# Kernel optimization log

Measured on AMD Instinct MI355X. Metric: run time of the kernel, lower is better.

The kernel has to match this reference:

```python
import jax, jax.numpy as jnp
import numpy as np

B, S, D = 1, 2048, 4096
H, DN, DR, DV = 16, 128, 64, 128        # heads, nope dim, rope dim, v dim
QLORA, KVLORA = 1536, 512
IN_, ID_, TOPK = 16, 128, 1024          # indexer heads, indexer head dim, top-k
NEG = -1e30


def _rope_interleaved(x, cos, sin):
    # pairs (x0,x1) interleaved as complex: used for MLA q/k rope parts
    xr, xi = x[..., 0::2], x[..., 1::2]
    yr = xr * cos - xi * sin
    yi = xr * sin + xi * cos
    return jnp.stack([yr, yi], axis=-1).reshape(x.shape)


def _rope_noninterleaved(x, cos, sin):
    # first half real, second half imaginary (indexer rope)
    h = x.shape[-1] // 2
    xr, xi = x[..., :h], x[..., h:]
    return jnp.concatenate([xr * cos - xi * sin, xr * sin + xi * cos], axis=-1)


def _rmsnorm(x, w, eps=1e-6):
    v = jnp.mean(jnp.square(x), axis=-1, keepdims=True)
    return x * jax.lax.rsqrt(v + eps) * w


def _layernorm(x, w, b, eps=1e-5):
    mu = jnp.mean(x, axis=-1, keepdims=True)
    var = jnp.mean(jnp.square(x - mu), axis=-1, keepdims=True)
    return (x - mu) * jax.lax.rsqrt(var + eps) * w + b


def setup_inputs() -> dict:
    key = jax.random.key(0)
    ks = jax.random.split(key, 9)
    def w(k, shape):
        return jax.random.normal(k, shape, jnp.float32) * 0.02
    hidden_states = jax.random.normal(ks[0], (B, S, D), jnp.float32)
    w_q_a = w(ks[1], (D, QLORA))
    w_q_b = w(ks[2], (QLORA, H * (DN + DR)))
    w_kv_a = w(ks[3], (D, KVLORA + DR))
    w_kv_b = w(ks[4], (KVLORA, H * (DN + DV)))
    w_o = w(ks[5], (H * DV, D))
    idx_wq_b = w(ks[6], (QLORA, IN_ * ID_))
    idx_wk = w(ks[7], (D, ID_))
    idx_w_proj = w(ks[8], (D, IN_))
    q_a_ln_w = jnp.ones((QLORA,), jnp.float32)
    kv_a_ln_w = jnp.ones((KVLORA,), jnp.float32)
    idx_k_ln_w = jnp.ones((ID_,), jnp.float32)
    idx_k_ln_b = jnp.zeros((ID_,), jnp.float32)
    inv_freq = 1.0 / (10000.0 ** (np.arange(0, DR, 2) / DR))
    ang = np.arange(S)[:, None] * inv_freq[None, :]  # [S, DR//2]
    cos = jnp.asarray(np.cos(ang), jnp.float32)
    sin = jnp.asarray(np.sin(ang), jnp.float32)
    return dict(hidden_states=hidden_states, cos=cos, sin=sin, w_q_a=w_q_a,
                q_a_ln_w=q_a_ln_w, w_q_b=w_q_b, w_kv_a=w_kv_a, kv_a_ln_w=kv_a_ln_w,
                w_kv_b=w_kv_b, w_o=w_o, idx_wq_b=idx_wq_b, idx_wk=idx_wk,
                idx_k_ln_w=idx_k_ln_w, idx_k_ln_b=idx_k_ln_b, idx_w_proj=idx_w_proj)


def reference(hidden_states, cos, sin, w_q_a, q_a_ln_w, w_q_b, w_kv_a, kv_a_ln_w,
              w_kv_b, w_o, idx_wq_b, idx_wk, idx_k_ln_w, idx_k_ln_b, idx_w_proj):
    b, s, _ = hidden_states.shape
    cos3, sin3 = cos[None, :, :], sin[None, :, :]          # [1, s, DR/2]
    cos4, sin4 = cos[None, :, None, :], sin[None, :, None, :]  # per-head broadcast

    # ---- MLA projections ----
    cq = _rmsnorm(hidden_states @ w_q_a, q_a_ln_w)          # [b,s,QLORA]
    q = (cq @ w_q_b).reshape(b, s, H, DN + DR)
    q_nope, q_rope = q[..., :DN], q[..., DN:]
    q_rope = _rope_interleaved(q_rope, cos4, sin4)
    kv = hidden_states @ w_kv_a                             # [b,s,KVLORA+DR]
    kv_c = _rmsnorm(kv[..., :KVLORA], kv_a_ln_w)
    k_rope = _rope_interleaved(kv[..., KVLORA:], cos3, sin3)  # shared (MQA) [b,s,DR]
    kvb = (kv_c @ w_kv_b).reshape(b, s, H, DN + DV)
    k_nope, v = kvb[..., :DN], kvb[..., DN:]

    causal = jnp.tril(jnp.ones((s, s), bool))

    # ---- lightning indexer (top-k token selection) ----
    qi = (cq @ idx_wq_b).reshape(b, s, IN_, ID_)
    qi = jnp.concatenate([_rope_noninterleaved(qi[..., :DR], cos4, sin4), qi[..., DR:]], -1)
    ki = _layernorm(hidden_states @ idx_wk, idx_k_ln_w, idx_k_ln_b)  # [b,s,ID_]
    ki = jnp.concatenate([_rope_noninterleaved(ki[..., :DR], cos3, sin3), ki[..., DR:]], -1)
    # NOTE: hadamard_transform_activation falls back to identity (no package) -> identity here
    wts = (hidden_states @ idx_w_proj) * (IN_ ** -0.5)       # [b,s,IN_]
    iscores = jax.nn.relu(jnp.einsum('bqnd,bkd->bqnk', qi, ki) * (ID_ ** -0.5))
    iscores = jnp.einsum('bqnk,bqn->bqk', iscores, wts)
    iscores = jnp.where(causal[None], iscores, NEG)
    _, topk_idx = jax.lax.top_k(iscores, TOPK)               # [b,s,TOPK]
    topk_mask = jnp.zeros((b, s, s), bool).at[
        jnp.arange(b)[:, None, None], jnp.arange(s)[None, :, None], topk_idx].set(True)
    allowed = topk_mask & causal[None]                       # [b,s,s]

    # ---- sparse MLA attention ----
    scale = (DN + DR) ** -0.5
    scores = (jnp.einsum('bqhd,bkhd->bhqk', q_nope, k_nope)
              + jnp.einsum('bqhd,bkd->bhqk', q_rope, k_rope)) * scale
    scores = jnp.where(allowed[:, None], scores, NEG)
    probs = jax.nn.softmax(scores, axis=-1)
    attn = jnp.einsum('bhqk,bkhd->bqhd', probs, v)
    return attn.reshape(b, s, H * DV) @ w_o
```

## Files before the change

kernel.cpp:

```cpp
#include <hip/hip_runtime.h>
#include <math.h>

#define S_LEN 2048
#define D_MODEL 4096
#define NH 16
#define TOPK_ 1024

typedef float f32x4 __attribute__((ext_vector_type(4)));
typedef short bf16x8 __attribute__((ext_vector_type(8)));

__device__ __forceinline__ unsigned short f2bf(float f) {
  unsigned u = __float_as_uint(f);
  u += 0x7fffu + ((u >> 16) & 1u);
  return (unsigned short)(u >> 16);
}

__device__ __forceinline__ void gload16(const unsigned short* g, unsigned short* l) {
  __builtin_amdgcn_global_load_lds(
      (const __attribute__((address_space(1))) unsigned int*)g,
      (__attribute__((address_space(3))) unsigned int*)l, 16, 0, 0);
}

__global__ __launch_bounds__(256) void gemm_bf16x(const unsigned short* __restrict__ A,
                                                  const unsigned short* __restrict__ Bt,
                                                  float* __restrict__ C,
                                                  int K, int lda, int ldb, int ldc,
                                                  int za, int zb, int zc) {
  A += (size_t)blockIdx.z * za;
  Bt += (size_t)blockIdx.z * zb;
  C += (size_t)blockIdx.z * zc;
  __shared__ __align__(16) unsigned short As[128 * 32];
  __shared__ __align__(16) unsigned short Bs[128 * 32];
  const int t = threadIdx.x, lane = t & 63, w = t >> 6;
  const int m0 = blockIdx.y * 128, n0 = blockIdx.x * 128;
  const int mb = (w & 1) * 64, nb = (w >> 1) * 64;
  const int fr = lane & 15, fq = lane >> 4;
  f32x4 acc[4][4];
#pragma unroll
  for (int i = 0; i < 4; i++)
#pragma unroll
    for (int j = 0; j < 4; j++) acc[i][j] = (f32x4){0.f, 0.f, 0.f, 0.f};
  const int grow = t >> 2, gsub = (t & 3) * 8;
  unsigned short* aswL = &As[w * 512];
  unsigned short* aswH = &As[2048 + w * 512];
  unsigned short* bswL = &Bs[w * 512];
  unsigned short* bswH = &Bs[2048 + w * 512];
  const unsigned short* AgL = A + (size_t)(m0 + grow) * lda + gsub;
  const unsigned short* AgH = A + (size_t)(m0 + 64 + grow) * lda + gsub;
  const unsigned short* BgL = Bt + (size_t)(n0 + grow) * ldb + gsub;
  const unsigned short* BgH = Bt + (size_t)(n0 + 64 + grow) * ldb + gsub;
  for (int k0 = 0; k0 < K; k0 += 32) {
    __syncthreads();
    gload16(AgL + k0, aswL);
    gload16(AgH + k0, aswH);
    gload16(BgL + k0, bswL);
    gload16(BgH + k0, bswH);
    __syncthreads();
    bf16x8 af[4], bfr[4];
#pragma unroll
    for (int mt = 0; mt < 4; mt++) af[mt] = *(const bf16x8*)&As[(mb + mt * 16 + fr) * 32 + fq * 8];
#pragma unroll
    for (int nt = 0; nt < 4; nt++) bfr[nt] = *(const bf16x8*)&Bs[(nb + nt * 16 + fr) * 32 + fq * 8];
#pragma unroll
    for (int mt = 0; mt < 4; mt++)
#pragma unroll
      for (int nt = 0; nt < 4; nt++)
        acc[mt][nt] = __builtin_amdgcn_mfma_f32_16x16x32_bf16(af[mt], bfr[nt], acc[mt][nt], 0, 0, 0);
  }
#pragma unroll
  for (int mt = 0; mt < 4; mt++) {
#pragma unroll
    for (int r = 0; r < 4; r++) {
      int row = m0 + mb + mt * 16 + fq * 4 + r;
      float* cp = C + (size_t)row * ldc + n0 + nb + fr;
#pragma unroll
      for (int nt = 0; nt < 4; nt++) cp[nt * 16] = acc[mt][nt][r];
    }
  }
}

__global__ __launch_bounds__(256) void gemm_bf16x_bf(const unsigned short* __restrict__ A,
                                                     const unsigned short* __restrict__ Bt,
                                                     unsigned short* __restrict__ C,
                                                     int K, int lda, int ldb, int ldc,
                                                     int za, int zb, int zc, float scale) {
  A += (size_t)blockIdx.z * za;
  Bt += (size_t)blockIdx.z * zb;
  C += (size_t)blockIdx.z * zc;
  __shared__ __align__(16) unsigned short As[128 * 32];
  __shared__ __align__(16) unsigned short Bs[128 * 32];
  const int t = threadIdx.x, lane = t & 63, w = t >> 6;
  const int m0 = blockIdx.y * 128, n0 = blockIdx.x * 128;
  const int mb = (w & 1) * 64, nb = (w >> 1) * 64;
  const int fr = lane & 15, fq = lane >> 4;
  f32x4 acc[4][4];
#pragma unroll
  for (int i = 0; i < 4; i++)
#pragma unroll
    for (int j = 0; j < 4; j++) acc[i][j] = (f32x4){0.f, 0.f, 0.f, 0.f};
  const int grow = t >> 2, gsub = (t & 3) * 8;
  unsigned short* aswL = &As[w * 512];
  unsigned short* aswH = &As[2048 + w * 512];
  unsigned short* bswL = &Bs[w * 512];
  unsigned short* bswH = &Bs[2048 + w * 512];
  const unsigned short* AgL = A + (size_t)(m0 + grow) * lda + gsub;
  const unsigned short* AgH = A + (size_t)(m0 + 64 + grow) * lda + gsub;
  const unsigned short* BgL = Bt + (size_t)(n0 + grow) * ldb + gsub;
  const unsigned short* BgH = Bt + (size_t)(n0 + 64 + grow) * ldb + gsub;
  for (int k0 = 0; k0 < K; k0 += 32) {
    __syncthreads();
    gload16(AgL + k0, aswL);
    gload16(AgH + k0, aswH);
    gload16(BgL + k0, bswL);
    gload16(BgH + k0, bswH);
    __syncthreads();
    bf16x8 af[4], bfr[4];
#pragma unroll
    for (int mt = 0; mt < 4; mt++) af[mt] = *(const bf16x8*)&As[(mb + mt * 16 + fr) * 32 + fq * 8];
#pragma unroll
    for (int nt = 0; nt < 4; nt++) bfr[nt] = *(const bf16x8*)&Bs[(nb + nt * 16 + fr) * 32 + fq * 8];
#pragma unroll
    for (int mt = 0; mt < 4; mt++)
#pragma unroll
      for (int nt = 0; nt < 4; nt++)
        acc[mt][nt] = __builtin_amdgcn_mfma_f32_16x16x32_bf16(af[mt], bfr[nt], acc[mt][nt], 0, 0, 0);
  }
#pragma unroll
  for (int mt = 0; mt < 4; mt++) {
#pragma unroll
    for (int r = 0; r < 4; r++) {
      int row = m0 + mb + mt * 16 + fq * 4 + r;
      unsigned short* cp = C + (size_t)row * ldc + n0 + nb + fr;
#pragma unroll
      for (int nt = 0; nt < 4; nt++) cp[nt * 16] = f2bf(acc[mt][nt][r] * scale);
    }
  }
}

__global__ __launch_bounds__(256) void cast_bf16(const float* __restrict__ in,
                                                 unsigned short* __restrict__ out) {
  size_t i = (size_t)(blockIdx.x * 256 + threadIdx.x) * 8;
  float4 v0 = *(const float4*)(in + i);
  float4 v1 = *(const float4*)(in + i + 4);
  unsigned short tmp[8] = {f2bf(v0.x), f2bf(v0.y), f2bf(v0.z), f2bf(v0.w),
                           f2bf(v1.x), f2bf(v1.y), f2bf(v1.z), f2bf(v1.w)};
  *(float4*)(out + i) = *(float4*)tmp;
}

__global__ __launch_bounds__(256) void transpose_cast(const float* __restrict__ in,
                                                      unsigned short* __restrict__ out,
                                                      int K, int N) {
  __shared__ float buf[64][33];
  const int k0 = blockIdx.y * 64, n0 = blockIdx.x * 32;
  const int t = threadIdx.x;
  const bool valid = (n0 < N);
  if (valid) {
#pragma unroll
    for (int i = 0; i < 2; i++) {
      int c = i * 256 + t;
      int kk = c >> 3, nn = (c & 7) * 4;
      float4 v = *(const float4*)(in + (size_t)(k0 + kk) * N + n0 + nn);
      buf[kk][nn] = v.x; buf[kk][nn + 1] = v.y; buf[kk][nn + 2] = v.z; buf[kk][nn + 3] = v.w;
    }
  }
  __syncthreads();
  const int n = t >> 3, k8 = (t & 7) * 8;
  unsigned short tmp[8];
#pragma unroll
  for (int j = 0; j < 8; j++) tmp[j] = valid ? f2bf(buf[k8 + j][n]) : (unsigned short)0;
  *(float4*)(out + (size_t)(n0 + n) * K + k0 + k8) = *(float4*)tmp;
}

__global__ __launch_bounds__(256) void transpose_wv(const unsigned short* __restrict__ wkvbbf,
                                                    unsigned short* __restrict__ wvT) {
  __shared__ unsigned short tile[128][136];
  const int c0 = blockIdx.x * 128, h = blockIdx.y;
  const int t = threadIdx.x;
  for (int i = t; i < 128 * 16; i += 256) {
    int c = i >> 4, sub = (i & 15) * 8;
    *(float4*)&tile[c][sub] = *(const float4*)(wkvbbf + (size_t)(c0 + c) * 4096 + h * 256 + 128 + sub);
  }
  __syncthreads();
  for (int i = t; i < 128 * 16; i += 256) {
    int d = i >> 4, cs = (i & 15) * 8;
    unsigned short tmp[8];
#pragma unroll
    for (int j = 0; j < 8; j++) tmp[j] = tile[cs + j][d];
    *(float4*)(wvT + (size_t)h * 65536 + (size_t)d * 512 + c0 + cs) = *(float4*)tmp;
  }
}

__global__ __launch_bounds__(256) void rmsnorm_kernel(float* __restrict__ x,
                                                      const float* __restrict__ w,
                                                      int ncol, int stride) {
  const int s = blockIdx.x, t = threadIdx.x;
  float* row = x + (size_t)s * stride;
  float ss = 0.f;
  for (int d = t; d < ncol; d += 256) { float v = row[d]; ss += v * v; }
  __shared__ float red[256];
  red[t] = ss;
  __syncthreads();
  for (int o = 128; o > 0; o >>= 1) { if (t < o) red[t] += red[t + o]; __syncthreads(); }
  float r = 1.0f / sqrtf(red[0] / (float)ncol + 1e-6f);
  for (int d = t; d < ncol; d += 256) row[d] = row[d] * r * w[d];
}

__global__ __launch_bounds__(256) void rmsnorm_bf16_kernel(float* __restrict__ x,
                                                           const float* __restrict__ w,
                                                           unsigned short* __restrict__ xbf,
                                                           int ncol, int stride) {
  const int s = blockIdx.x, t = threadIdx.x;
  float* row = x + (size_t)s * stride;
  float ss = 0.f;
  for (int d = t; d < ncol; d += 256) { float v = row[d]; ss += v * v; }
  __shared__ float red[256];
  red[t] = ss;
  __syncthreads();
  for (int o = 128; o > 0; o >>= 1) { if (t < o) red[t] += red[t + o]; __syncthreads(); }
  float r = 1.0f / sqrtf(red[0] / (float)ncol + 1e-6f);
  for (int d = t; d < ncol; d += 256) {
    float v = row[d] * r * w[d];
    row[d] = v;
    xbf[(size_t)s * ncol + d] = f2bf(v);
  }
}

__global__ __launch_bounds__(128) void layernorm128_kernel(float* __restrict__ x,
                                                           const float* __restrict__ w,
                                                           const float* __restrict__ b) {
  const int s = blockIdx.x, t = threadIdx.x;
  float* row = x + (size_t)s * 128;
  __shared__ float red[128];
  float v = row[t];
  red[t] = v;
  __syncthreads();
  for (int o = 64; o > 0; o >>= 1) { if (t < o) red[t] += red[t + o]; __syncthreads(); }
  float mu = red[0] / 128.f;
  __syncthreads();
  float d = v - mu;
  red[t] = d * d;
  __syncthreads();
  for (int o = 64; o > 0; o >>= 1) { if (t < o) red[t] += red[t + o]; __syncthreads(); }
  float var = red[0] / 128.f;
  row[t] = d * (1.0f / sqrtf(var + 1e-5f)) * w[t] + b[t];
}

__global__ __launch_bounds__(256) void rope_q_inter(float* __restrict__ q,
                                                    const float* __restrict__ cosp,
                                                    const float* __restrict__ sinp) {
  int id = blockIdx.x * 256 + threadIdx.x;
  int s = id >> 9, r = id & 511, h = r >> 5, j = r & 31;
  float c = cosp[s * 32 + j], sn = sinp[s * 32 + j];
  float* base = q + (size_t)s * (NH * 192) + h * 192 + 128 + 2 * j;
  float x0 = base[0], x1 = base[1];
  base[0] = x0 * c - x1 * sn;
  base[1] = x0 * sn + x1 * c;
}

__global__ __launch_bounds__(256) void rope_k_inter(float* __restrict__ kv,
                                                    const float* __restrict__ cosp,
                                                    const float* __restrict__ sinp,
                                                    int stride) {
  int id = blockIdx.x * 256 + threadIdx.x;
  int s = id >> 5, j = id & 31;
  float c = cosp[s * 32 + j], sn = sinp[s * 32 + j];
  float* base = kv + (size_t)s * stride + 512 + 2 * j;
  float x0 = base[0], x1 = base[1];
  base[0] = x0 * c - x1 * sn;
  base[1] = x0 * sn + x1 * c;
}

__global__ __launch_bounds__(256) void rope_qi_nonint(float* __restrict__ qi,
                                                      const float* __restrict__ cosp,
                                                      const float* __restrict__ sinp) {
  int id = blockIdx.x * 256 + threadIdx.x;
  int s = id >> 9, r = id & 511, n = r >> 5, j = r & 31;
  float c = cosp[s * 32 + j], sn = sinp[s * 32 + j];
  float* base = qi + (size_t)s * 2048 + n * 128;
  float xr = base[j], xi = base[j + 32];
  base[j] = xr * c - xi * sn;
  base[j + 32] = xr * sn + xi * c;
}

__global__ __launch_bounds__(256) void rope_ki_nonint(float* __restrict__ ki,
                                                      const float* __restrict__ cosp,
                                                      const float* __restrict__ sinp) {
  int id = blockIdx.x * 256 + threadIdx.x;
  int s = id >> 5, j = id & 31;
  float c = cosp[s * 32 + j], sn = sinp[s * 32 + j];
  float* base = ki + (size_t)s * 128;
  float xr = base[j], xi = base[j + 32];
  base[j] = xr * c - xi * sn;
  base[j + 32] = xr * sn + xi * c;
}

__global__ __launch_bounds__(256) void wts_kernel(const float* __restrict__ hs,
                                                  const float* __restrict__ wp,
                                                  float* __restrict__ wts) {
  const int s = blockIdx.x, t = threadIdx.x;
  float acc[16] = {};
  for (int d = t; d < D_MODEL; d += 256) {
    float h = hs[(size_t)s * D_MODEL + d];
    const float* w = wp + (size_t)d * 16;
#pragma unroll
    for (int n = 0; n < 16; n++) acc[n] += h * w[n];
  }
  __shared__ float red[16][256];
#pragma unroll
  for (int n = 0; n < 16; n++) red[n][t] = acc[n];
  __syncthreads();
  for (int o = 128; o > 0; o >>= 1) {
    if (t < o) {
#pragma unroll
      for (int n = 0; n < 16; n++) red[n][t] += red[n][t + o];
    }
    __syncthreads();
  }
  if (t < 16) wts[(size_t)s * 16 + t] = red[t][0] * 0.022097086912079613f;
}

__global__ __launch_bounds__(256) void indexer_mfma(const unsigned short* __restrict__ qibf,
                                                    const unsigned short* __restrict__ kibf,
                                                    const float* __restrict__ wts,
                                                    float* __restrict__ isc) {
  __shared__ unsigned short kis[64 * 136];
  __shared__ unsigned short qis[64 * 136];
  __shared__ float wt_s[64 * 16];
  const int t = threadIdx.x, lane = t & 63, w = t >> 6;
  const int ln = lane & 15, quad = lane >> 4;
  int b = blockIdx.x;
  int qt = (int)((sqrtf(8.0f * b + 1.0f) - 1.0f) * 0.5f);
  while ((qt + 1) * (qt + 2) / 2 <= b) qt++;
  while (qt * (qt + 1) / 2 > b) qt--;
  const int kt = b - qt * (qt + 1) / 2;
  const int q0 = qt * 64, k0 = kt * 64;
#pragma unroll
  for (int p = 0; p < 4; p++) {
    int i = t + p * 256;
    int row = i >> 4, sub = (i & 15) * 8;
    *(float4*)&kis[row * 136 + sub] = *(const float4*)(kibf + (size_t)(k0 + row) * 128 + sub);
  }
  {
    int rw = t >> 2, n4 = (t & 3) * 4;
    *(float4*)&wt_s[rw * 16 + n4] = *(const float4*)(wts + (size_t)(q0 + rw) * 16 + n4);
  }
  __syncthreads();
  bf16x8 kb[4][4];
#pragma unroll
  for (int nt = 0; nt < 4; nt++)
#pragma unroll
    for (int kk = 0; kk < 4; kk++)
      kb[nt][kk] = *(const bf16x8*)&kis[(nt * 16 + ln) * 136 + kk * 32 + quad * 8];
  f32x4 iacc[4];
#pragma unroll
  for (int nt = 0; nt < 4; nt++) iacc[nt] = (f32x4){0.f, 0.f, 0.f, 0.f};

  for (int n = 0; n < 16; n++) {
    __syncthreads();
#pragma unroll
    for (int p = 0; p < 4; p++) {
      int i = t + p * 256;
      int row = i >> 4, sub = (i & 15) * 8;
      *(float4*)&qis[row * 136 + sub] =
          *(const float4*)(qibf + (size_t)(q0 + row) * 2048 + n * 128 + sub);
    }
    __syncthreads();
    bf16x8 qa[4];
#pragma unroll
    for (int kk = 0; kk < 4; kk++)
      qa[kk] = *(const bf16x8*)&qis[(w * 16 + ln) * 136 + kk * 32 + quad * 8];
    float wv0 = wt_s[(w * 16 + quad * 4 + 0) * 16 + n];
    float wv1 = wt_s[(w * 16 + quad * 4 + 1) * 16 + n];
    float wv2 = wt_s[(w * 16 + quad * 4 + 2) * 16 + n];
    float wv3 = wt_s[(w * 16 + quad * 4 + 3) * 16 + n];
#pragma unroll
    for (int nt = 0; nt < 4; nt++) {
      f32x4 sacc = (f32x4){0.f, 0.f, 0.f, 0.f};
#pragma unroll
      for (int kk = 0; kk < 4; kk++)
        sacc = __builtin_amdgcn_mfma_f32_16x16x32_bf16(qa[kk], kb[nt][kk], sacc, 0, 0, 0);
      iacc[nt][0] += fmaxf(sacc[0], 0.f) * wv0;
      iacc[nt][1] += fmaxf(sacc[1], 0.f) * wv1;
      iacc[nt][2] += fmaxf(sacc[2], 0.f) * wv2;
      iacc[nt][3] += fmaxf(sacc[3], 0.f) * wv3;
    }
  }
#pragma unroll
  for (int nt = 0; nt < 4; nt++) {
#pragma unroll
    for (int r = 0; r < 4; r++) {
      int qg = q0 + w * 16 + quad * 4 + r;
      int kg = k0 + nt * 16 + ln;
      isc[(size_t)qg * 2048 + kg] = (kg <= qg) ? iacc[nt][r] : -1.0e30f;
    }
  }
}

__global__ __launch_bounds__(256) void topk_select(const float* __restrict__ sc,
                                                   int* __restrict__ sel,
                                                   int* __restrict__ selcnt) {
  const int s = blockIdx.x, t = threadIdx.x;
  if (s < TOPK_) {
    for (int k = t; k <= s; k += 256) sel[(size_t)s * TOPK_ + k] = k;
    if (t == 0) selcnt[s] = s + 1;
    return;
  }
  __shared__ unsigned keys[2048];
  __shared__ unsigned hist[256];
  __shared__ unsigned sh_prefix, sh_K, sh_cnt;
  const int L = s + 1;
  for (int k = t; k < L; k += 256) {
    unsigned u = __float_as_uint(sc[(size_t)s * 2048 + k]);
    u = (u & 0x80000000u) ? ~u : (u | 0x80000000u);
    keys[k] = u;
  }
  if (t == 0) { sh_prefix = 0u; sh_K = TOPK_; sh_cnt = 0u; }
  __syncthreads();
#pragma unroll
  for (int pass = 0; pass < 4; pass++) {
    const int shift = 24 - 8 * pass;
    const unsigned mask_hi = (pass == 0) ? 0u : (0xFFFFFFFFu << (shift + 8));
    hist[t] = 0u;
    __syncthreads();
    unsigned prefix = sh_prefix;
    for (int k = t; k < L; k += 256) {
      unsigned u = keys[k];
      if ((u & mask_hi) == prefix) atomicAdd(&hist[(u >> shift) & 255u], 1u);
    }
    __syncthreads();
    if (t == 0) {
      unsigned K = sh_K, cum = 0u;
      int b = 255;
      for (; b >= 0; b--) {
        cum += hist[b];
        if (cum >= K) break;
      }
      sh_K = K - (cum - hist[b]);
      sh_prefix = prefix | ((unsigned)b << shift);
    }
    __syncthreads();
  }
  const unsigned T = sh_prefix;
  const unsigned Keq = sh_K;
  for (int k = t; k < L; k += 256) {
    if (keys[k] > T) {
      unsigned p = atomicAdd(&sh_cnt, 1u);
      sel[(size_t)s * TOPK_ + p] = k;
    }
  }
  __syncthreads();
  if (t == 0) {
    unsigned base = sh_cnt, taken = 0u;
    for (int k = 0; k < L && taken < Keq; k++) {
      if (keys[k] == T) { sel[(size_t)s * TOPK_ + base + taken] = k; taken++; }
    }
    selcnt[s] = TOPK_;
  }
}

__global__ __launch_bounds__(256) void kv_to_bf16_pad(const float* __restrict__ kvp,
                                                      unsigned short* __restrict__ kvbf) {
  const int s = blockIdx.x, t = threadIdx.x;
  for (int c = t; c < 576; c += 256)
    kvbf[(size_t)s * 576 + c] = f2bf(kvp[(size_t)s * 640 + c]);
}

__global__ __launch_bounds__(256) void qfull_rope(const float* __restrict__ qb,
                                                  unsigned short* __restrict__ qfull) {
  int id = blockIdx.x * 256 + threadIdx.x;
  int s = id >> 9, r = id & 511, h = r >> 5, j = r & 31;
  const float qscale = 0.07216878364870322f;
  const float* src = qb + (size_t)s * 3072 + h * 192 + 128 + 2 * j;
  unsigned pk = (unsigned)f2bf(src[0] * qscale) | ((unsigned)f2bf(src[1] * qscale) << 16);
  *(unsigned*)(qfull + (size_t)s * 9216 + h * 576 + 512 + 2 * j) = pk;
}

#define KC 32
__global__ __launch_bounds__(256, 3) void flash_attn2(const unsigned short* __restrict__ qfull,
                                                      const unsigned short* __restrict__ kvbf,
                                                      const int* __restrict__ sel,
                                                      unsigned short* __restrict__ o_c) {
  const int s = blockIdx.x, t = threadIdx.x;
  const int lane = t & 63, w = t >> 6;
  const int half = w >> 1, kt = w & 1;
  const int ln = lane & 15, quad = lane >> 4;
  __shared__ unsigned kvt2[288 * 36];
  __shared__ float s_part[2][16][36];
  __shared__ unsigned short p_bf[16][40];
  __shared__ float al_sh[16], l_sh[16];
  const int cnt = (s < 1024) ? (s + 1) : 1024;

  bf16x8 qa[9];
  {
    const unsigned short* qrow = qfull + (size_t)s * 9216 + ln * 576 + half * 288 + quad * 8;
#pragma unroll
    for (int kk = 0; kk < 9; kk++) qa[kk] = *(const bf16x8*)(qrow + kk * 32);
  }
  f32x4 o[8];
#pragma unroll
  for (int i = 0; i < 8; i++) o[i] = (f32x4){0.f, 0.f, 0.f, 0.f};
  float m_run = -3.0e38f, l_run = 0.f;
  const int skey = t >> 3, ssub = t & 7;
  const int scol = skey ^ ((ssub & 3) << 3);
  const int keyi = (kt * 16 + ln) ^ (quad << 3);
  const int pvoff = (quad ^ ((ln >> 2) & 3)) << 3;

  float4 pf[9];
  bool vld;
  {
    int gk = skey;
    vld = (gk < cnt);
    if (vld) {
      const unsigned short* sp = kvbf + (size_t)sel[(size_t)s * TOPK_ + gk] * 576;
#pragma unroll
      for (int j = 0; j < 9; j++) pf[j] = *(const float4*)(sp + (ssub + 8 * j) * 8);
    }
  }

  for (int k0 = 0; k0 < cnt; k0 += KC) {
    __syncthreads();
    if (vld) {
#pragma unroll
      for (int j = 0; j < 9; j++) {
        const unsigned* pv = (const unsigned*)&pf[j];
        int base = ((ssub + 8 * j) * 4) * 36 + scol;
        kvt2[base] = pv[0];
        kvt2[base + 36] = pv[1];
        kvt2[base + 72] = pv[2];
        kvt2[base + 108] = pv[3];
      }
    } else {
#pragma unroll
      for (int j = 0; j < 9; j++) {
        int base = ((ssub + 8 * j) * 4) * 36 + scol;
        kvt2[base] = 0u; kvt2[base + 36] = 0u; kvt2[base + 72] = 0u; kvt2[base + 108] = 0u;
      }
    }
    {
      int gkn = k0 + KC + skey;
      bool vn = (gkn < cnt);
      if (vn) {
        const unsigned short* sp = kvbf + (size_t)sel[(size_t)s * TOPK_ + gkn] * 576;
#pragma unroll
        for (int j = 0; j < 9; j++) pf[j] = *(const float4*)(sp + (ssub + 8 * j) * 8);
      }
      vld = vn;
    }
    __syncthreads();
    {
      f32x4 sacc = (f32x4){0.f, 0.f, 0.f, 0.f};
#pragma unroll
      for (int kk = 0; kk < 9; kk++) {
        int c2b = half * 144 + kk * 16 + quad * 4;
        unsigned bw[4];
        bw[0] = kvt2[c2b * 36 + keyi];
        bw[1] = kvt2[(c2b + 1) * 36 + keyi];
        bw[2] = kvt2[(c2b + 2) * 36 + keyi];
        bw[3] = kvt2[(c2b + 3) * 36 + keyi];
        sacc = __builtin_amdgcn_mfma_f32_16x16x32_bf16(qa[kk], *(const bf16x8*)bw, sacc, 0, 0, 0);
      }
#pragma unroll
      for (int r = 0; r < 4; r++) s_part[half][quad * 4 + r][kt * 16 + ln] = sacc[r];
    }
    __syncthreads();
    {
      const int h = w * 4 + quad;
      float a0 = s_part[0][h][2 * ln] + s_part[1][h][2 * ln];
      float a1 = s_part[0][h][2 * ln + 1] + s_part[1][h][2 * ln + 1];
      float v0 = (k0 + 2 * ln < cnt) ? a0 : -3.0e38f;
      float v1 = (k0 + 2 * ln + 1 < cnt) ? a1 : -3.0e38f;
      float tm = fmaxf(v0, v1);
      tm = fmaxf(tm, __shfl_xor(tm, 1));
      tm = fmaxf(tm, __shfl_xor(tm, 2));
      tm = fmaxf(tm, __shfl_xor(tm, 4));
      tm = fmaxf(tm, __shfl_xor(tm, 8));
      float mn = fmaxf(m_run, tm);
      float alpha = __expf(m_run - mn);
      m_run = mn;
      float p0 = __expf(v0 - mn);
      float p1 = __expf(v1 - mn);
      unsigned pk = (unsigned)f2bf(p0) | ((unsigned)f2bf(p1) << 16);
      *(unsigned*)&p_bf[h][2 * ln] = pk;
      float rs = p0 + p1;
      rs += __shfl_xor(rs, 1);
      rs += __shfl_xor(rs, 2);
      rs += __shfl_xor(rs, 4);
      rs += __shfl_xor(rs, 8);
      l_run = l_run * alpha + rs;
      if (ln == 0) al_sh[h] = alpha;
    }
    __syncthreads();
    {
      bf16x8 pa = *(const bf16x8*)&p_bf[ln][quad * 8];
      float al0 = al_sh[quad * 4 + 0], al1 = al_sh[quad * 4 + 1];
      float al2 = al_sh[quad * 4 + 2], al3 = al_sh[quad * 4 + 3];
#pragma unroll
      for (int i = 0; i < 8; i++) {
        o[i][0] *= al0; o[i][1] *= al1; o[i][2] *= al2; o[i][3] *= al3;
      }
#pragma unroll
      for (int tau = 0; tau < 4; tau++) {
        const unsigned* kp = &kvt2[(w * 64 + tau * 16 + ln) * 36 + pvoff];
        uint4 lo = *(const uint4*)kp;
        uint4 hi = *(const uint4*)(kp + 4);
        unsigned ev[4], od[4];
        ev[0] = __builtin_amdgcn_perm(lo.y, lo.x, 0x05040100u);
        od[0] = __builtin_amdgcn_perm(lo.y, lo.x, 0x07060302u);
        ev[1] = __builtin_amdgcn_perm(lo.w, lo.z, 0x05040100u);
        od[1] = __builtin_amdgcn_perm(lo.w, lo.z, 0x07060302u);
        ev[2] = __builtin_amdgcn_perm(hi.y, hi.x, 0x05040100u);
        od[2] = __builtin_amdgcn_perm(hi.y, hi.x, 0x07060302u);
        ev[3] = __builtin_amdgcn_perm(hi.w, hi.z, 0x05040100u);
        od[3] = __builtin_amdgcn_perm(hi.w, hi.z, 0x07060302u);
        o[tau * 2]     = __builtin_amdgcn_mfma_f32_16x16x32_bf16(pa, *(const bf16x8*)ev, o[tau * 2], 0, 0, 0);
        o[tau * 2 + 1] = __builtin_amdgcn_mfma_f32_16x16x32_bf16(pa, *(const bf16x8*)od, o[tau * 2 + 1], 0, 0, 0);
      }
    }
  }
  if (ln == 0) l_sh[w * 4 + quad] = 1.0f / l_run;
  __syncthreads();
  {
    float li[4] = {l_sh[quad * 4 + 0], l_sh[quad * 4 + 1], l_sh[quad * 4 + 2], l_sh[quad * 4 + 3]};
#pragma unroll
    for (int tau = 0; tau < 4; tau++) {
      int c2 = w * 64 + tau * 16 + ln;
#pragma unroll
      for (int r = 0; r < 4; r++) {
        int h = quad * 4 + r;
        unsigned pk = (unsigned)f2bf(o[tau * 2][r] * li[r]) |
                      ((unsigned)f2bf(o[tau * 2 + 1][r] * li[r]) << 16);
        *(unsigned*)(o_c + (size_t)s * 8192 + h * 512 + 2 * c2) = pk;
      }
    }
  }
}

extern "C" void kernel_launch(void* const* d_in, const int* in_sizes, int n_in,
                              void* d_out, int out_size, void* d_ws, size_t ws_size,
                              hipStream_t stream) {
  const float* hs         = (const float*)d_in[0];
  const float* cosp       = (const float*)d_in[1];
  const float* sinp       = (const float*)d_in[2];
  const float* w_q_a      = (const float*)d_in[3];
  const float* q_a_ln_w   = (const float*)d_in[4];
  const float* w_q_b      = (const float*)d_in[5];
  const float* w_kv_a     = (const float*)d_in[6];
  const float* kv_a_ln_w  = (const float*)d_in[7];
  const float* w_kv_b     = (const float*)d_in[8];
  const float* w_o        = (const float*)d_in[9];
  const float* idx_wq_b   = (const float*)d_in[10];
  const float* idx_wk     = (const float*)d_in[11];
  const float* idx_k_ln_w = (const float*)d_in[12];
  const float* idx_k_ln_b = (const float*)d_in[13];
  const float* idx_w_proj = (const float*)d_in[14];
  float* out = (float*)d_out;

  float* ws = (float*)d_ws;
  float*          qb      = ws;
  float*          cq      = ws + 6291456;
  unsigned short* qbbf    = (unsigned short*)cq;
  unsigned short* cqbf    = (unsigned short*)(ws + 9437184);
  float*          kvp     = ws + 11010048;
  unsigned short* kvbf    = (unsigned short*)(ws + 12320768);
  float*          wts     = ws + 12910592;
  int*            sel     = (int*)(ws + 12943360);
  int*            selcnt  = sel + 2097152;
  float*          ki      = ws + 15042560;
  unsigned short* kibf    = (unsigned short*)(ws + 15304704);
  unsigned short* wkvbbf  = (unsigned short*)(ws + 15435776);
  unsigned short* wvT     = (unsigned short*)(ws + 16484352);
  unsigned short* attnbbf = (unsigned short*)(ws + 17008640);
  unsigned short* o_c     = (unsigned short*)(ws + 19105792);
  unsigned short* woT     = o_c;
  unsigned short* hsbf    = (unsigned short*)(ws + 27494400);
  float*          qi      = ws + 31688704;
  unsigned short* qibf    = (unsigned short*)(ws + 35883008);
  float*          isc     = ws + 37980160;
  unsigned short* qfull   = (unsigned short*)qi;
  unsigned short* wT      = (unsigned short*)(ws + 42174464);

  const float qscale = 0.07216878364870322f;

  cast_bf16<<<4096, 256, 0, stream>>>(hs, hsbf);
  transpose_cast<<<dim3(48, 64), 256, 0, stream>>>(w_q_a, wT, 4096, 1536);
  gemm_bf16x<<<dim3(12, 16, 1), 256, 0, stream>>>(hsbf, wT, cq, 4096, 4096, 4096, 1536, 0, 0, 0);
  rmsnorm_bf16_kernel<<<2048, 256, 0, stream>>>(cq, q_a_ln_w, cqbf, 1536, 1536);

  transpose_cast<<<dim3(64, 24), 256, 0, stream>>>(idx_wq_b, wT, 1536, 2048);
  gemm_bf16x<<<dim3(16, 16, 1), 256, 0, stream>>>(cqbf, wT, qi, 1536, 1536, 1536, 2048, 0, 0, 0);
  rope_qi_nonint<<<4096, 256, 0, stream>>>(qi, cosp, sinp);
  cast_bf16<<<2048, 256, 0, stream>>>(qi, qibf);
  transpose_cast<<<dim3(4, 64), 256, 0, stream>>>(idx_wk, wT, 4096, 128);
  gemm_bf16x<<<dim3(1, 16, 1), 256, 0, stream>>>(hsbf, wT, ki, 4096, 4096, 4096, 128, 0, 0, 0);
  layernorm128_kernel<<<2048, 128, 0, stream>>>(ki, idx_k_ln_w, idx_k_ln_b);
  rope_ki_nonint<<<256, 256, 0, stream>>>(ki, cosp, sinp);
  cast_bf16<<<128, 256, 0, stream>>>(ki, kibf);
  wts_kernel<<<2048, 256, 0, stream>>>(hs, idx_w_proj, wts);
  indexer_mfma<<<528, 256, 0, stream>>>(qibf, kibf, wts, isc);
  topk_select<<<2048, 256, 0, stream>>>(isc, sel, selcnt);

  transpose_cast<<<dim3(96, 24), 256, 0, stream>>>(w_q_b, wT, 1536, 3072);
  gemm_bf16x<<<dim3(24, 16, 1), 256, 0, stream>>>(cqbf, wT, qb, 1536, 1536, 1536, 3072, 0, 0, 0);
  rope_q_inter<<<4096, 256, 0, stream>>>(qb, cosp, sinp);
  cast_bf16<<<3072, 256, 0, stream>>>(qb, qbbf);

  transpose_cast<<<dim3(20, 64), 256, 0, stream>>>(w_kv_a, wT, 4096, 576);
  gemm_bf16x<<<dim3(5, 16, 1), 256, 0, stream>>>(hsbf, wT, kvp, 4096, 4096, 4096, 640, 0, 0, 0);
  rmsnorm_kernel<<<2048, 256, 0, stream>>>(kvp, kv_a_ln_w, 512, 640);
  rope_k_inter<<<256, 256, 0, stream>>>(kvp, cosp, sinp, 640);
  kv_to_bf16_pad<<<2048, 256, 0, stream>>>(kvp, kvbf);

  cast_bf16<<<1024, 256, 0, stream>>>(w_kv_b, wkvbbf);
  gemm_bf16x_bf<<<dim3(4, 16, 16), 256, 0, stream>>>(qbbf, wkvbbf, qfull,
                                                     128, 3072, 4096, 9216, 192, 256, 576, qscale);
  qfull_rope<<<4096, 256, 0, stream>>>(qb, qfull);

  flash_attn2<<<2048, 256, 0, stream>>>(qfull, kvbf, sel, o_c);

  transpose_wv<<<dim3(4, 16), 256, 0, stream>>>(wkvbbf, wvT);
  gemm_bf16x_bf<<<dim3(1, 16, 16), 256, 0, stream>>>(o_c, wvT, attnbbf,
                                                     512, 8192, 512, 2048, 512, 65536, 128, 1.0f);

  transpose_cast<<<dim3(128, 32), 256, 0, stream>>>(w_o, woT, 2048, 4096);
  gemm_bf16x<<<dim3(32, 16, 1), 256, 0, stream>>>(attnbbf, woT, out, 2048, 2048, 2048, 4096, 0, 0, 0);
}
```

Baseline: 1.138 ms.

## Double-buffer GEMM LDS tiles and split-K the skinny projection GEMMs

The bf16 MFMA GEMM kernels now use two LDS buffers, so the next K-tile's global-to-LDS load is issued before the current tile's MFMAs instead of behind a barrier. A new split-K GEMM kernel accumulates partial sums with atomicAdd into zeroed outputs. It is used for the three low-occupancy GEMMs on hidden_states (q_a, indexer k, kv_a) so they launch more blocks. The cost is extra memsets, atomic traffic, doubled LDS per block, and non-deterministic float summation order.

```diff
diff --git a/kernel.cpp b/kernel.cpp
--- a/kernel.cpp
+++ b/kernel.cpp
@@ -29,8 +29,8 @@
   A += (size_t)blockIdx.z * za;
   Bt += (size_t)blockIdx.z * zb;
   C += (size_t)blockIdx.z * zc;
-  __shared__ __align__(16) unsigned short As[128 * 32];
-  __shared__ __align__(16) unsigned short Bs[128 * 32];
+  __shared__ __align__(16) unsigned short As[2][128 * 32];
+  __shared__ __align__(16) unsigned short Bs[2][128 * 32];
   const int t = threadIdx.x, lane = t & 63, w = t >> 6;
   const int m0 = blockIdx.y * 128, n0 = blockIdx.x * 128;
   const int mb = (w & 1) * 64, nb = (w >> 1) * 64;
@@ -41,31 +41,35 @@
 #pragma unroll
     for (int j = 0; j < 4; j++) acc[i][j] = (f32x4){0.f, 0.f, 0.f, 0.f};
   const int grow = t >> 2, gsub = (t & 3) * 8;
-  unsigned short* aswL = &As[w * 512];
-  unsigned short* aswH = &As[2048 + w * 512];
-  unsigned short* bswL = &Bs[w * 512];
-  unsigned short* bswH = &Bs[2048 + w * 512];
+  const int wb = w * 512;
   const unsigned short* AgL = A + (size_t)(m0 + grow) * lda + gsub;
   const unsigned short* AgH = A + (size_t)(m0 + 64 + grow) * lda + gsub;
   const unsigned short* BgL = Bt + (size_t)(n0 + grow) * ldb + gsub;
   const unsigned short* BgH = Bt + (size_t)(n0 + 64 + grow) * ldb + gsub;
+  gload16(AgL, &As[0][wb]);
+  gload16(AgH, &As[0][2048 + wb]);
+  gload16(BgL, &Bs[0][wb]);
+  gload16(BgH, &Bs[0][2048 + wb]);
+  int cur = 0;
   for (int k0 = 0; k0 < K; k0 += 32) {
     __syncthreads();
-    gload16(AgL + k0, aswL);
-    gload16(AgH + k0, aswH);
-    gload16(BgL + k0, bswL);
-    gload16(BgH + k0, bswH);
-    __syncthreads();
+    if (k0 + 32 < K) {
+      gload16(AgL + k0 + 32, &As[cur ^ 1][wb]);
+      gload16(AgH + k0 + 32, &As[cur ^ 1][2048 + wb]);
+      gload16(BgL + k0 + 32, &Bs[cur ^ 1][wb]);
+      gload16(BgH + k0 + 32, &Bs[cur ^ 1][2048 + wb]);
+    }
     bf16x8 af[4], bfr[4];
 #pragma unroll
-    for (int mt = 0; mt < 4; mt++) af[mt] = *(const bf16x8*)&As[(mb + mt * 16 + fr) * 32 + fq * 8];
-#pragma unroll
-    for (int nt = 0; nt < 4; nt++) bfr[nt] = *(const bf16x8*)&Bs[(nb + nt * 16 + fr) * 32 + fq * 8];
+    for (int mt = 0; mt < 4; mt++) af[mt] = *(const bf16x8*)&As[cur][(mb + mt * 16 + fr) * 32 + fq * 8];
+#pragma unroll
+    for (int nt = 0; nt < 4; nt++) bfr[nt] = *(const bf16x8*)&Bs[cur][(nb + nt * 16 + fr) * 32 + fq * 8];
 #pragma unroll
     for (int mt = 0; mt < 4; mt++)
 #pragma unroll
       for (int nt = 0; nt < 4; nt++)
         acc[mt][nt] = __builtin_amdgcn_mfma_f32_16x16x32_bf16(af[mt], bfr[nt], acc[mt][nt], 0, 0, 0);
+    cur ^= 1;
   }
 #pragma unroll
   for (int mt = 0; mt < 4; mt++) {
@@ -87,8 +91,8 @@
   A += (size_t)blockIdx.z * za;
   Bt += (size_t)blockIdx.z * zb;
   C += (size_t)blockIdx.z * zc;
-  __shared__ __align__(16) unsigned short As[128 * 32];
-  __shared__ __align__(16) unsigned short Bs[128 * 32];
+  __shared__ __align__(16) unsigned short As[2][128 * 32];
+  __shared__ __align__(16) unsigned short Bs[2][128 * 32];
   const int t = threadIdx.x, lane = t & 63, w = t >> 6;
   const int m0 = blockIdx.y * 128, n0 = blockIdx.x * 128;
   const int mb = (w & 1) * 64, nb = (w >> 1) * 64;
@@ -99,31 +103,35 @@
 #pragma unroll
     for (int j = 0; j < 4; j++) acc[i][j] = (f32x4){0.f, 0.f, 0.f, 0.f};
   const int grow = t >> 2, gsub = (t & 3) * 8;
-  unsigned short* aswL = &As[w * 512];
-  unsigned short* aswH = &As[2048 + w * 512];
-  unsigned short* bswL = &Bs[w * 512];
-  unsigned short* bswH = &Bs[2048 + w * 512];
+  const int wb = w * 512;
   const unsigned short* AgL = A + (size_t)(m0 + grow) * lda + gsub;
   const unsigned short* AgH = A + (size_t)(m0 + 64 + grow) * lda + gsub;
   const unsigned short* BgL = Bt + (size_t)(n0 + grow) * ldb + gsub;
   const unsigned short* BgH = Bt + (size_t)(n0 + 64 + grow) * ldb + gsub;
+  gload16(AgL, &As[0][wb]);
+  gload16(AgH, &As[0][2048 + wb]);
+  gload16(BgL, &Bs[0][wb]);
+  gload16(BgH, &Bs[0][2048 + wb]);
+  int cur = 0;
   for (int k0 = 0; k0 < K; k0 += 32) {
     __syncthreads();
-    gload16(AgL + k0, aswL);
-    gload16(AgH + k0, aswH);
-    gload16(BgL + k0, bswL);
-    gload16(BgH + k0, bswH);
-    __syncthreads();
+    if (k0 + 32 < K) {
+      gload16(AgL + k0 + 32, &As[cur ^ 1][wb]);
+      gload16(AgH + k0 + 32, &As[cur ^ 1][2048 + wb]);
+      gload16(BgL + k0 + 32, &Bs[cur ^ 1][wb]);
+      gload16(BgH + k0 + 32, &Bs[cur ^ 1][2048 + wb]);
+    }
     bf16x8 af[4], bfr[4];
 #pragma unroll
-    for (int mt = 0; mt < 4; mt++) af[mt] = *(const bf16x8*)&As[(mb + mt * 16 + fr) * 32 + fq * 8];
-#pragma unroll
-    for (int nt = 0; nt < 4; nt++) bfr[nt] = *(const bf16x8*)&Bs[(nb + nt * 16 + fr) * 32 + fq * 8];
+    for (int mt = 0; mt < 4; mt++) af[mt] = *(const bf16x8*)&As[cur][(mb + mt * 16 + fr) * 32 + fq * 8];
+#pragma unroll
+    for (int nt = 0; nt < 4; nt++) bfr[nt] = *(const bf16x8*)&Bs[cur][(nb + nt * 16 + fr) * 32 + fq * 8];
 #pragma unroll
     for (int mt = 0; mt < 4; mt++)
 #pragma unroll
       for (int nt = 0; nt < 4; nt++)
         acc[mt][nt] = __builtin_amdgcn_mfma_f32_16x16x32_bf16(af[mt], bfr[nt], acc[mt][nt], 0, 0, 0);
+    cur ^= 1;
   }
 #pragma unroll
   for (int mt = 0; mt < 4; mt++) {
@@ -133,6 +141,65 @@
       unsigned short* cp = C + (size_t)row * ldc + n0 + nb + fr;
 #pragma unroll
       for (int nt = 0; nt < 4; nt++) cp[nt * 16] = f2bf(acc[mt][nt][r] * scale);
+    }
+  }
+}
+
+__global__ __launch_bounds__(256) void gemm_bf16x_sk(const unsigned short* __restrict__ A,
+                                                     const unsigned short* __restrict__ Bt,
+                                                     float* __restrict__ C,
+                                                     int Kc, int lda, int ldb, int ldc) {
+  const int kbase = blockIdx.z * Kc;
+  __shared__ __align__(16) unsigned short As[2][128 * 32];
+  __shared__ __align__(16) unsigned short Bs[2][128 * 32];
+  const int t = threadIdx.x, lane = t & 63, w = t >> 6;
+  const int m0 = blockIdx.y * 128, n0 = blockIdx.x * 128;
+  const int mb = (w & 1) * 64, nb = (w >> 1) * 64;
+  const int fr = lane & 15, fq = lane >> 4;
+  f32x4 acc[4][4];
+#pragma unroll
+  for (int i = 0; i < 4; i++)
+#pragma unroll
+    for (int j = 0; j < 4; j++) acc[i][j] = (f32x4){0.f, 0.f, 0.f, 0.f};
+  const int grow = t >> 2, gsub = (t & 3) * 8;
+  const int wb = w * 512;
+  const unsigned short* AgL = A + (size_t)(m0 + grow) * lda + kbase + gsub;
+  const unsigned short* AgH = A + (size_t)(m0 + 64 + grow) * lda + kbase + gsub;
+  const unsigned short* BgL = Bt + (size_t)(n0 + grow) * ldb + kbase + gsub;
+  const unsigned short* BgH = Bt + (size_t)(n0 + 64 + grow) * ldb + kbase + gsub;
+  gload16(AgL, &As[0][wb]);
+  gload16(AgH, &As[0][2048 + wb]);
+  gload16(BgL, &Bs[0][wb]);
+  gload16(BgH, &Bs[0][2048 + wb]);
+  int cur = 0;
+  for (int k0 = 0; k0 < Kc; k0 += 32) {
+    __syncthreads();
+    if (k0 + 32 < Kc) {
+      gload16(AgL + k0 + 32, &As[cur ^ 1][wb]);
+      gload16(AgH + k0 + 32, &As[cur ^ 1][2048 + wb]);
+      gload16(BgL + k0 + 32, &Bs[cur ^ 1][wb]);
+      gload16(BgH + k0 + 32, &Bs[cur ^ 1][2048 + wb]);
+    }
+    bf16x8 af[4], bfr[4];
+#pragma unroll
+    for (int mt = 0; mt < 4; mt++) af[mt] = *(const bf16x8*)&As[cur][(mb + mt * 16 + fr) * 32 + fq * 8];
+#pragma unroll
+    for (int nt = 0; nt < 4; nt++) bfr[nt] = *(const bf16x8*)&Bs[cur][(nb + nt * 16 + fr) * 32 + fq * 8];
+#pragma unroll
+    for (int mt = 0; mt < 4; mt++)
+#pragma unroll
+      for (int nt = 0; nt < 4; nt++)
+        acc[mt][nt] = __builtin_amdgcn_mfma_f32_16x16x32_bf16(af[mt], bfr[nt], acc[mt][nt], 0, 0, 0);
+    cur ^= 1;
+  }
+#pragma unroll
+  for (int mt = 0; mt < 4; mt++) {
+#pragma unroll
+    for (int r = 0; r < 4; r++) {
+      int row = m0 + mb + mt * 16 + fq * 4 + r;
+      float* cp = C + (size_t)row * ldc + n0 + nb + fr;
+#pragma unroll
+      for (int nt = 0; nt < 4; nt++) atomicAdd(cp + nt * 16, acc[mt][nt][r]);
     }
   }
 }
@@ -683,7 +750,8 @@
 
   cast_bf16<<<4096, 256, 0, stream>>>(hs, hsbf);
   transpose_cast<<<dim3(48, 64), 256, 0, stream>>>(w_q_a, wT, 4096, 1536);
-  gemm_bf16x<<<dim3(12, 16, 1), 256, 0, stream>>>(hsbf, wT, cq, 4096, 4096, 4096, 1536, 0, 0, 0);
+  hipMemsetAsync(cq, 0, (size_t)2048 * 1536 * 4, stream);
+  gemm_bf16x_sk<<<dim3(12, 16, 2), 256, 0, stream>>>(hsbf, wT, cq, 2048, 4096, 4096, 1536);
   rmsnorm_bf16_kernel<<<2048, 256, 0, stream>>>(cq, q_a_ln_w, cqbf, 1536, 1536);
 
   transpose_cast<<<dim3(64, 24), 256, 0, stream>>>(idx_wq_b, wT, 1536, 2048);
@@ -691,7 +759,8 @@
   rope_qi_nonint<<<4096, 256, 0, stream>>>(qi, cosp, sinp);
   cast_bf16<<<2048, 256, 0, stream>>>(qi, qibf);
   transpose_cast<<<dim3(4, 64), 256, 0, stream>>>(idx_wk, wT, 4096, 128);
-  gemm_bf16x<<<dim3(1, 16, 1), 256, 0, stream>>>(hsbf, wT, ki, 4096, 4096, 4096, 128, 0, 0, 0);
+  hipMemsetAsync(ki, 0, (size_t)2048 * 128 * 4, stream);
+  gemm_bf16x_sk<<<dim3(1, 16, 8), 256, 0, stream>>>(hsbf, wT, ki, 512, 4096, 4096, 128);
   layernorm128_kernel<<<2048, 128, 0, stream>>>(ki, idx_k_ln_w, idx_k_ln_b);
   rope_ki_nonint<<<256, 256, 0, stream>>>(ki, cosp, sinp);
   cast_bf16<<<128, 256, 0, stream>>>(ki, kibf);
@@ -705,7 +774,8 @@
   cast_bf16<<<3072, 256, 0, stream>>>(qb, qbbf);
 
   transpose_cast<<<dim3(20, 64), 256, 0, stream>>>(w_kv_a, wT, 4096, 576);
-  gemm_bf16x<<<dim3(5, 16, 1), 256, 0, stream>>>(hsbf, wT, kvp, 4096, 4096, 4096, 640, 0, 0, 0);
+  hipMemsetAsync(kvp, 0, (size_t)2048 * 640 * 4, stream);
+  gemm_bf16x_sk<<<dim3(5, 16, 4), 256, 0, stream>>>(hsbf, wT, kvp, 1024, 4096, 4096, 640);
   rmsnorm_kernel<<<2048, 256, 0, stream>>>(kvp, kv_a_ln_w, 512, 640);
   rope_k_inter<<<256, 256, 0, stream>>>(kvp, cosp, sinp, 640);
   kv_to_bf16_pad<<<2048, 256, 0, stream>>>(kvp, kvbf);
```

Result: faster. 970.3 us (-14.7%).
